# Kernel optimization log

Measured on AMD Instinct MI355X. Metric: run time of the kernel, lower is better.

The kernel has to match this reference:

```python
import jax, jax.numpy as jnp
import numpy as np

N = 100000
E = 1000000
HID = 64


def gcn_conv(x, W, b, edge_index, edge_w, num_nodes):
    # PyG GCNConv with edge_weight: add self-loops (weight 1), symmetric norm,
    # out[c] = sum_e norm_e * (x @ W)[row_e] aggregated at col_e, plus bias.
    xw = x @ W  # [N, hid]
    row = jnp.concatenate([edge_index[0], jnp.arange(num_nodes)])
    col = jnp.concatenate([edge_index[1], jnp.arange(num_nodes)])
    ew = jnp.concatenate([edge_w, jnp.ones((num_nodes,), x.dtype)])
    deg = jax.ops.segment_sum(ew, col, num_segments=num_nodes)
    dinv = jnp.where(deg > 0, jax.lax.rsqrt(deg), 0.0)
    norm = dinv[row] * ew * dinv[col]  # [E+N]
    msgs = norm[:, None] * xw[row]  # [E+N, hid]
    out = jax.ops.segment_sum(msgs, col, num_segments=num_nodes)
    return out + b


def setup_inputs() -> dict:
    key = jax.random.key(0)
    ks = jax.random.split(key, 12)
    user_x = jax.random.normal(ks[0], (N, 3), jnp.float32)
    movie_x = jax.random.normal(ks[1], (N, 18), jnp.float32)
    edge_index = jax.random.randint(ks[2], (2, E), 0, N, jnp.int64)
    edge_attr = jax.random.uniform(ks[3], (E,), jnp.float32)
    def lin(k, fan_in, fan_out):
        bound = 1.0 / np.sqrt(fan_in)
        k1, k2 = jax.random.split(k)
        W = jax.random.uniform(k1, (fan_in, fan_out), jnp.float32, -bound, bound)
        b = jax.random.uniform(k2, (fan_out,), jnp.float32, -bound, bound)
        return W, b
    W_user, b_user = lin(ks[4], 3, HID)
    W_movie, b_movie = lin(ks[5], 18, HID)
    W1, b1 = lin(ks[6], 2 * HID, 128)
    W2, b2 = lin(ks[7], 128, 1)
    return {"user_x": user_x, "movie_x": movie_x, "edge_index": edge_index,
            "edge_attr": edge_attr, "W_user": W_user, "b_user": b_user,
            "W_movie": W_movie, "b_movie": b_movie, "W1": W1, "b1": b1,
            "W2": W2, "b2": b2}


def reference(user_x, movie_x, edge_index, edge_attr, W_user, b_user,
              W_movie, b_movie, W1, b1, W2, b2):
    user_out = gcn_conv(user_x, W_user, b_user, edge_index, edge_attr, N)
    movie_out = gcn_conv(movie_x, W_movie, b_movie, edge_index, edge_attr, N)
    h = jnp.concatenate([user_out, movie_out], axis=-1)  # [N, 128]
    h = jax.nn.relu(h @ W1 + b1)
    rating_pred = h @ W2 + b2  # [N, 1]
    return rating_pred
```

## Files before the change

kernel.cpp:

```cpp
#include <hip/hip_runtime.h>
#include <hip/hip_fp16.h>

#define NN 100000
#define NE 1000000
#define BSH 7
#define BCOLS 128
#define NBUCK 782
#define SBLK 256
#define SITER 16
#define CAP 2048

__device__ __forceinline__ float2 h2f(unsigned u) {
    union { unsigned u; __half2 h; } c; c.u = u;
    return __half22float2(c.h);
}
__device__ __forceinline__ unsigned f2h2(float a, float b) {
    union { __half2 h; unsigned u; } c; c.h = __floats2half2_rn(a, b);
    return c.u;
}

#define ACC_ROW16(base)                                                      \
    {                                                                        \
        const uint4* pr_ = (const uint4*)(base);                             \
        const uint4 A_ = pr_[0];                                             \
        const uint4 B_ = pr_[1];                                             \
        const uint4 C_ = pr_[2];                                             \
        float2 f_;                                                           \
        f_ = h2f(A_.x); s21[0]  = fmaf(w, f_.x, s21[0]);  s21[1]  = fmaf(w, f_.y, s21[1]);  \
        f_ = h2f(A_.y); s21[2]  = fmaf(w, f_.x, s21[2]);  s21[3]  = fmaf(w, f_.y, s21[3]);  \
        f_ = h2f(A_.z); s21[4]  = fmaf(w, f_.x, s21[4]);  s21[5]  = fmaf(w, f_.y, s21[5]);  \
        f_ = h2f(A_.w); s21[6]  = fmaf(w, f_.x, s21[6]);  s21[7]  = fmaf(w, f_.y, s21[7]);  \
        f_ = h2f(B_.x); s21[8]  = fmaf(w, f_.x, s21[8]);  s21[9]  = fmaf(w, f_.y, s21[9]);  \
        f_ = h2f(B_.y); s21[10] = fmaf(w, f_.x, s21[10]); s21[11] = fmaf(w, f_.y, s21[11]); \
        f_ = h2f(B_.z); s21[12] = fmaf(w, f_.x, s21[12]); s21[13] = fmaf(w, f_.y, s21[13]); \
        f_ = h2f(B_.w); s21[14] = fmaf(w, f_.x, s21[14]); s21[15] = fmaf(w, f_.y, s21[15]); \
        f_ = h2f(C_.x); s21[16] = fmaf(w, f_.x, s21[16]); s21[17] = fmaf(w, f_.y, s21[17]); \
        f_ = h2f(C_.y); s21[18] = fmaf(w, f_.x, s21[18]); s21[19] = fmaf(w, f_.y, s21[19]); \
        f_ = h2f(C_.z); s21[20] = fmaf(w, f_.x, s21[20]);                    \
    }

__global__ __launch_bounds__(128) void fuse_kernel(const float* __restrict__ Wu,
                                                   const float* __restrict__ bu,
                                                   const float* __restrict__ Wm,
                                                   const float* __restrict__ bm,
                                                   const float* __restrict__ W1,
                                                   const float* __restrict__ b1,
                                                   const float* __restrict__ W2,
                                                   float* __restrict__ Mt,
                                                   int* __restrict__ cnt) {
    const int j = threadIdx.x;
    for (int i = j; i < NBUCK; i += 128) cnt[i] = 0;

    float w1c[128];
#pragma unroll
    for (int k = 0; k < 128; k++) w1c[k] = W1[k * 128 + j];

    float* row = Mt + j * 24;
#pragma unroll
    for (int m = 0; m < 3; m++) {
        float acc = 0.f;
#pragma unroll
        for (int k = 0; k < 64; k++) acc = fmaf(Wu[m * 64 + k], w1c[k], acc);
        row[m] = acc;
    }
#pragma unroll
    for (int m = 0; m < 18; m++) {
        float acc = 0.f;
#pragma unroll
        for (int k = 0; k < 64; k++) acc = fmaf(Wm[m * 64 + k], w1c[64 + k], acc);
        row[3 + m] = acc;
    }
    float bp = b1[j];
#pragma unroll
    for (int k = 0; k < 64; k++) {
        bp = fmaf(bu[k], w1c[k], bp);
        bp = fmaf(bm[k], w1c[64 + k], bp);
    }
    row[21] = bp;
    row[22] = W2[j];
    row[23] = 0.f;
}

__global__ __launch_bounds__(256) void bcnt_kernel(const int* __restrict__ col,
                                                   int* __restrict__ cnt) {
    __shared__ int h[NBUCK];
    for (int i = threadIdx.x; i < NBUCK; i += 256) h[i] = 0;
    __syncthreads();
    for (int e = blockIdx.x * 256 + threadIdx.x; e < NE; e += SBLK * 256)
        atomicAdd(&h[col[e] >> BSH], 1);
    __syncthreads();
    for (int i = threadIdx.x; i < NBUCK; i += 256)
        if (h[i]) atomicAdd(&cnt[i], h[i]);
}

__global__ __launch_bounds__(1024) void bscan_kernel(const int* __restrict__ cnt,
                                                     int* __restrict__ gbase,
                                                     int* __restrict__ H0) {
    __shared__ int s[1024];
    const int t = threadIdx.x;
    const int v = (t < NBUCK) ? cnt[t] : 0;
    s[t] = v;
    __syncthreads();
    for (int off = 1; off < 1024; off <<= 1) {
        int x = (t >= off) ? s[t - off] : 0;
        __syncthreads();
        s[t] += x;
        __syncthreads();
    }
    const int excl = s[t] - v;
    if (t < NBUCK) { gbase[t] = excl; H0[t] = excl; }
    if (t == 0) H0[NBUCK] = NE;
}

__global__ __launch_bounds__(256) void bscatter_kernel(const int* __restrict__ ei,
                                                       const float* __restrict__ ew,
                                                       int* __restrict__ gbase,
                                                       int2* __restrict__ mid) {
    __shared__ int h[NBUCK];
    __shared__ int rbase[NBUCK];
    int cs[SITER], rs[SITER];
    float wv[SITER];
    const int e0 = blockIdx.x * 256 + threadIdx.x;

    for (int i = threadIdx.x; i < NBUCK; i += 256) h[i] = 0;
    __syncthreads();
#pragma unroll
    for (int k = 0; k < SITER; k++) {
        const int e = e0 + k * (SBLK * 256);
        if (e < NE) {
            cs[k] = ei[NE + e];
            rs[k] = ei[e];
            wv[k] = ew[e];
            atomicAdd(&h[cs[k] >> BSH], 1);
        }
    }
    __syncthreads();
    for (int i = threadIdx.x; i < NBUCK; i += 256) {
        const int c0 = h[i];
        rbase[i] = c0 ? atomicAdd(&gbase[i], c0) : 0;
        h[i] = 0;
    }
    __syncthreads();
#pragma unroll
    for (int k = 0; k < SITER; k++) {
        const int e = e0 + k * (SBLK * 256);
        if (e < NE) {
            const int bb = cs[k] >> BSH;
            const int pos = rbase[bb] + atomicAdd(&h[bb], 1);
            mid[pos] = make_int2((cs[k] & (BCOLS - 1)) | (rs[k] << BSH),
                                 __float_as_int(wv[k]));
        }
    }
}

__global__ __launch_bounds__(256) void bdeg_pack_kernel(const int2* __restrict__ mid,
                                                        const int* __restrict__ H0,
                                                        const float* __restrict__ ux,
                                                        const float* __restrict__ mx,
                                                        unsigned short* __restrict__ pack16,
                                                        float* __restrict__ dinv) {
    __shared__ float dl[BCOLS];
    const int b = blockIdx.x;
    const int t = threadIdx.x;
    if (t < BCOLS) dl[t] = 0.f;
    __syncthreads();
    const int start = H0[b];
    const int end = H0[b + 1];
    for (int i = start + t; i < end; i += 256) {
        const int2 p = mid[i];
        atomicAdd(&dl[p.x & (BCOLS - 1)], __int_as_float(p.y));
    }
    __syncthreads();
    if (t < BCOLS) {
        const int r = b * BCOLS + t;
        if (r < NN) {
            const float d = rsqrtf(dl[t] + 1.0f);
            dinv[r] = d;
            float v[22];
            const float* u = ux + (size_t)r * 3;
            const float* m = mx + (size_t)r * 18;
            v[0] = d * u[0];
            v[1] = d * u[1];
            v[2] = d * u[2];
#pragma unroll
            for (int k = 0; k < 18; k++) v[3 + k] = d * m[k];
            v[21] = d;
            unsigned wb[16];
#pragma unroll
            for (int k = 0; k < 11; k++) wb[k] = f2h2(v[2 * k], v[2 * k + 1]);
#pragma unroll
            for (int k = 11; k < 16; k++) wb[k] = 0u;
            uint4* dst = (uint4*)(pack16 + (size_t)r * 32);
            dst[0] = make_uint4(wb[0], wb[1], wb[2], wb[3]);
            dst[1] = make_uint4(wb[4], wb[5], wb[6], wb[7]);
            dst[2] = make_uint4(wb[8], wb[9], wb[10], wb[11]);
            dst[3] = make_uint4(wb[12], wb[13], wb[14], wb[15]);
        }
    }
}

__global__ __launch_bounds__(256) void bagg_mlp_kernel(const int2* __restrict__ mid,
                                                       const int* __restrict__ H0,
                                                       const unsigned short* __restrict__ pack16,
                                                       const float* __restrict__ dinv,
                                                       const float* __restrict__ Mt,
                                                       const float* __restrict__ b2,
                                                       float* __restrict__ out) {
    __shared__ int2 smid[CAP];
    __shared__ int ccnt[BCOLS];
    __shared__ int cbase[BCOLS];
    __shared__ int cptr[BCOLS];
    __shared__ float sp[BCOLS][21];
    __shared__ float po[BCOLS];

    const int b = blockIdx.x;
    const int t = threadIdx.x;
    const int col = t & (BCOLS - 1);
    const int hf = t >> 7;
    const int start = H0[b];
    const int end = H0[b + 1];
    const int seg = end - start;
    const int segc = seg < CAP ? seg : CAP;

    if (t < BCOLS) ccnt[t] = 0;
    __syncthreads();
    for (int i = t; i < segc; i += 256)
        atomicAdd(&ccnt[mid[start + i].x & (BCOLS - 1)], 1);
    __syncthreads();

    if (t < 64) {
        const int a = ccnt[2 * t];
        const int bb = ccnt[2 * t + 1];
        int p = a + bb;
#pragma unroll
        for (int d = 1; d < 64; d <<= 1) {
            const int x = __shfl_up(p, d, 64);
            if (t >= d) p += x;
        }
        cbase[2 * t] = p - bb;
        cbase[2 * t + 1] = p;
        cptr[2 * t] = p - bb - a;
        cptr[2 * t + 1] = p - bb;
    }
    __syncthreads();

    for (int i = t; i < segc; i += 256) {
        const int2 p = mid[start + i];
        const int pos = atomicAdd(&cptr[p.x & (BCOLS - 1)], 1);
        smid[pos] = p;
    }
    __syncthreads();

    float s21[21];
#pragma unroll
    for (int m = 0; m < 21; m++) s21[m] = 0.f;

    const int s0 = (col == 0) ? 0 : cbase[col - 1];
    const int s1 = cbase[col];
#pragma unroll 2
    for (int i = s0 + hf; i < s1; i += 2) {
        const int2 p = smid[i];
        const unsigned row = ((unsigned)p.x) >> BSH;
        const float w = __int_as_float(p.y);
        ACC_ROW16(pack16 + (size_t)row * 32);
    }

    if (hf) {
#pragma unroll
        for (int m = 0; m < 21; m++) sp[col][m] = s21[m];
    }
    __syncthreads();

    const int c = b * BCOLS + col;
    if (!hf) {
#pragma unroll
        for (int m = 0; m < 21; m++) s21[m] += sp[col][m];
        if (seg > CAP) {
            for (int i = CAP; i < seg; i++) {
                const int2 p = mid[start + i];
                if ((p.x & (BCOLS - 1)) == col) {
                    const unsigned row = ((unsigned)p.x) >> BSH;
                    const float w = __int_as_float(p.y);
                    ACC_ROW16(pack16 + (size_t)row * 32);
                }
            }
        }
        if (c < NN) {
            const float w = 1.0f;
            ACC_ROW16(pack16 + (size_t)c * 32);
            const float d = dinv[c];
#pragma unroll
            for (int m = 0; m < 21; m++) s21[m] *= d;
        }
#pragma unroll
        for (int m = 0; m < 21; m++) sp[col][m] = s21[m];
    }
    __syncthreads();
    if (hf) {
#pragma unroll
        for (int m = 0; m < 21; m++) s21[m] = sp[col][m];
    }

    float o = 0.f;
    const int k0 = hf * 64;
#pragma unroll 4
    for (int k = k0; k < k0 + 64; k++) {
        const float* r = Mt + k * 24;
        float hsum = r[21];
#pragma unroll
        for (int m = 0; m < 21; m++) hsum = fmaf(s21[m], r[m], hsum);
        o = fmaf(fmaxf(hsum, 0.f), r[22], o);
    }
    if (hf) po[col] = o;
    __syncthreads();
    if (!hf && c < NN) out[c] = o + po[col] + b2[0];
}

extern "C" void kernel_launch(void* const* d_in, const int* in_sizes, int n_in,
                              void* d_out, int out_size, void* d_ws, size_t ws_size,
                              hipStream_t stream) {
    const float* ux = (const float*)d_in[0];
    const float* mx = (const float*)d_in[1];
    const int* ei = (const int*)d_in[2];
    const float* ew = (const float*)d_in[3];
    const float* Wu = (const float*)d_in[4];
    const float* bu = (const float*)d_in[5];
    const float* Wm = (const float*)d_in[6];
    const float* bm = (const float*)d_in[7];
    const float* W1 = (const float*)d_in[8];
    const float* b1 = (const float*)d_in[9];
    const float* W2 = (const float*)d_in[10];
    const float* b2 = (const float*)d_in[11];
    float* out = (float*)d_out;

    char* ws = (char*)d_ws;
    int*            cnt    = (int*)ws;
    int*            gbase  = (int*)(ws + 4096);
    int*            H0     = (int*)(ws + 8192);
    float*          Mt     = (float*)(ws + 12288);
    float*          dinv   = (float*)(ws + 24576);
    unsigned short* pack16 = (unsigned short*)(ws + 424576);
    int2*           mid    = (int2*)(ws + 6824576);

    fuse_kernel<<<1, 128, 0, stream>>>(Wu, bu, Wm, bm, W1, b1, W2, Mt, cnt);
    bcnt_kernel<<<SBLK, 256, 0, stream>>>(ei + NE, cnt);
    bscan_kernel<<<1, 1024, 0, stream>>>(cnt, gbase, H0);
    bscatter_kernel<<<SBLK, 256, 0, stream>>>(ei, ew, gbase, mid);
    bdeg_pack_kernel<<<NBUCK, 256, 0, stream>>>(mid, H0, ux, mx, pack16, dinv);
    bagg_mlp_kernel<<<NBUCK, 256, 0, stream>>>(mid, H0, pack16, dinv, Mt, b2, out);
}
```

Baseline: 196.8 us.

## Stage bucket scatter in shared memory and compute degrees via global atomics

The degree sum moves into the bucket-count pass as global float atomics, with zeroing done by extra blocks of the fuse kernel, so the pack kernel no longer re-reads the bucketed edge list per bucket. The scatter kernel now sorts its edges by bucket in LDS with a local prefix scan before writing, so global writes to the mid buffer are contiguous runs instead of random scattered stores. The aggregation kernel caches its edge segment in registers instead of reading it twice from global memory. The cost is a million global float atomics in the count pass and much larger LDS use in the scatter kernel, about 50 KB, which lowers its occupancy.

```diff
diff --git a/kernel.cpp b/kernel.cpp
--- a/kernel.cpp
+++ b/kernel.cpp
@@ -8,6 +8,7 @@
 #define NBUCK 782
 #define SBLK 256
 #define SITER 16
+#define SEDG (SITER * 256)
 #define CAP 2048
 
 __device__ __forceinline__ float2 h2f(unsigned u) {
@@ -39,18 +40,23 @@
         f_ = h2f(C_.z); s21[20] = fmaf(w, f_.x, s21[20]);                    \
     }
 
-__global__ __launch_bounds__(128) void fuse_kernel(const float* __restrict__ Wu,
-                                                   const float* __restrict__ bu,
-                                                   const float* __restrict__ Wm,
-                                                   const float* __restrict__ bm,
-                                                   const float* __restrict__ W1,
-                                                   const float* __restrict__ b1,
-                                                   const float* __restrict__ W2,
-                                                   float* __restrict__ Mt,
-                                                   int* __restrict__ cnt) {
+__global__ __launch_bounds__(128) void fuse_zero_kernel(const float* __restrict__ Wu,
+                                                        const float* __restrict__ bu,
+                                                        const float* __restrict__ Wm,
+                                                        const float* __restrict__ bm,
+                                                        const float* __restrict__ W1,
+                                                        const float* __restrict__ b1,
+                                                        const float* __restrict__ W2,
+                                                        float* __restrict__ Mt,
+                                                        int* __restrict__ cnt,
+                                                        float* __restrict__ degf) {
+    if (blockIdx.x != 0) {
+        const int tid = (blockIdx.x - 1) * 128 + threadIdx.x;
+        for (int i = tid; i < NBUCK; i += 256 * 128) cnt[i] = 0;
+        for (int i = tid; i < NN; i += 256 * 128) degf[i] = 0.f;
+        return;
+    }
     const int j = threadIdx.x;
-    for (int i = j; i < NBUCK; i += 128) cnt[i] = 0;
-
     float w1c[128];
 #pragma unroll
     for (int k = 0; k < 128; k++) w1c[k] = W1[k * 128 + j];
@@ -82,12 +88,17 @@
 }
 
 __global__ __launch_bounds__(256) void bcnt_kernel(const int* __restrict__ col,
-                                                   int* __restrict__ cnt) {
+                                                   const float* __restrict__ ew,
+                                                   int* __restrict__ cnt,
+                                                   float* __restrict__ degf) {
     __shared__ int h[NBUCK];
     for (int i = threadIdx.x; i < NBUCK; i += 256) h[i] = 0;
     __syncthreads();
-    for (int e = blockIdx.x * 256 + threadIdx.x; e < NE; e += SBLK * 256)
-        atomicAdd(&h[col[e] >> BSH], 1);
+    for (int e = blockIdx.x * 256 + threadIdx.x; e < NE; e += SBLK * 256) {
+        const int c = col[e];
+        atomicAdd(&h[c >> BSH], 1);
+        atomicAdd(&degf[c], ew[e]);
+    }
     __syncthreads();
     for (int i = threadIdx.x; i < NBUCK; i += 256)
         if (h[i]) atomicAdd(&cnt[i], h[i]);
@@ -116,14 +127,24 @@
                                                        const float* __restrict__ ew,
                                                        int* __restrict__ gbase,
                                                        int2* __restrict__ mid) {
+    __shared__ int2 stage[SEDG];
+    __shared__ unsigned short sbk[SEDG];
     __shared__ int h[NBUCK];
+    __shared__ int basel[NBUCK];
+    __shared__ int cptr[NBUCK];
     __shared__ int rbase[NBUCK];
+    __shared__ int wtot[4];
+    __shared__ int wpre[4];
+    __shared__ int stot;
+
     int cs[SITER], rs[SITER];
     float wv[SITER];
-    const int e0 = blockIdx.x * 256 + threadIdx.x;
-
-    for (int i = threadIdx.x; i < NBUCK; i += 256) h[i] = 0;
-    __syncthreads();
+    const int t = threadIdx.x;
+    const int e0 = blockIdx.x * 256 + t;
+
+    for (int i = t; i < NBUCK; i += 256) h[i] = 0;
+    __syncthreads();
+
 #pragma unroll
     for (int k = 0; k < SITER; k++) {
         const int e = e0 + k * (SBLK * 256);
@@ -135,68 +156,98 @@
         }
     }
     __syncthreads();
-    for (int i = threadIdx.x; i < NBUCK; i += 256) {
+
+    int loc[4];
+    int tsum = 0;
+#pragma unroll
+    for (int j = 0; j < 4; j++) {
+        const int idx = t * 4 + j;
+        const int v = (idx < NBUCK) ? h[idx] : 0;
+        loc[j] = tsum;
+        tsum += v;
+    }
+    const int lane = t & 63;
+    const int wv_id = t >> 6;
+    int incl = tsum;
+#pragma unroll
+    for (int d = 1; d < 64; d <<= 1) {
+        const int x = __shfl_up(incl, d, 64);
+        if (lane >= d) incl += x;
+    }
+    if (lane == 63) wtot[wv_id] = incl;
+    __syncthreads();
+    if (t == 0) {
+        int r = 0;
+#pragma unroll
+        for (int i = 0; i < 4; i++) { wpre[i] = r; r += wtot[i]; }
+        stot = r;
+    }
+    __syncthreads();
+    const int texcl = incl - tsum + wpre[wv_id];
+#pragma unroll
+    for (int j = 0; j < 4; j++) {
+        const int idx = t * 4 + j;
+        if (idx < NBUCK) {
+            basel[idx] = texcl + loc[j];
+            cptr[idx] = texcl + loc[j];
+        }
+    }
+    __syncthreads();
+
+    for (int i = t; i < NBUCK; i += 256) {
         const int c0 = h[i];
         rbase[i] = c0 ? atomicAdd(&gbase[i], c0) : 0;
-        h[i] = 0;
-    }
-    __syncthreads();
+    }
+    __syncthreads();
+
 #pragma unroll
     for (int k = 0; k < SITER; k++) {
         const int e = e0 + k * (SBLK * 256);
         if (e < NE) {
             const int bb = cs[k] >> BSH;
-            const int pos = rbase[bb] + atomicAdd(&h[bb], 1);
-            mid[pos] = make_int2((cs[k] & (BCOLS - 1)) | (rs[k] << BSH),
-                                 __float_as_int(wv[k]));
-        }
-    }
-}
-
-__global__ __launch_bounds__(256) void bdeg_pack_kernel(const int2* __restrict__ mid,
-                                                        const int* __restrict__ H0,
-                                                        const float* __restrict__ ux,
-                                                        const float* __restrict__ mx,
-                                                        unsigned short* __restrict__ pack16,
-                                                        float* __restrict__ dinv) {
-    __shared__ float dl[BCOLS];
-    const int b = blockIdx.x;
-    const int t = threadIdx.x;
-    if (t < BCOLS) dl[t] = 0.f;
-    __syncthreads();
-    const int start = H0[b];
-    const int end = H0[b + 1];
-    for (int i = start + t; i < end; i += 256) {
-        const int2 p = mid[i];
-        atomicAdd(&dl[p.x & (BCOLS - 1)], __int_as_float(p.y));
-    }
-    __syncthreads();
-    if (t < BCOLS) {
-        const int r = b * BCOLS + t;
-        if (r < NN) {
-            const float d = rsqrtf(dl[t] + 1.0f);
-            dinv[r] = d;
-            float v[22];
-            const float* u = ux + (size_t)r * 3;
-            const float* m = mx + (size_t)r * 18;
-            v[0] = d * u[0];
-            v[1] = d * u[1];
-            v[2] = d * u[2];
-#pragma unroll
-            for (int k = 0; k < 18; k++) v[3 + k] = d * m[k];
-            v[21] = d;
-            unsigned wb[16];
-#pragma unroll
-            for (int k = 0; k < 11; k++) wb[k] = f2h2(v[2 * k], v[2 * k + 1]);
-#pragma unroll
-            for (int k = 11; k < 16; k++) wb[k] = 0u;
-            uint4* dst = (uint4*)(pack16 + (size_t)r * 32);
-            dst[0] = make_uint4(wb[0], wb[1], wb[2], wb[3]);
-            dst[1] = make_uint4(wb[4], wb[5], wb[6], wb[7]);
-            dst[2] = make_uint4(wb[8], wb[9], wb[10], wb[11]);
-            dst[3] = make_uint4(wb[12], wb[13], wb[14], wb[15]);
-        }
-    }
+            const int pos = atomicAdd(&cptr[bb], 1);
+            stage[pos] = make_int2((cs[k] & (BCOLS - 1)) | (rs[k] << BSH),
+                                   __float_as_int(wv[k]));
+            sbk[pos] = (unsigned short)bb;
+        }
+    }
+    __syncthreads();
+
+    const int tot = stot;
+    for (int i = t; i < tot; i += 256) {
+        const int bb = sbk[i];
+        mid[rbase[bb] + (i - basel[bb])] = stage[i];
+    }
+}
+
+__global__ __launch_bounds__(256) void pack_kernel(const float* __restrict__ degf,
+                                                   const float* __restrict__ ux,
+                                                   const float* __restrict__ mx,
+                                                   unsigned short* __restrict__ pack16,
+                                                   float* __restrict__ dinv) {
+    const int r = blockIdx.x * 256 + threadIdx.x;
+    if (r >= NN) return;
+    const float d = rsqrtf(degf[r] + 1.0f);
+    dinv[r] = d;
+    float v[22];
+    const float* u = ux + (size_t)r * 3;
+    const float* m = mx + (size_t)r * 18;
+    v[0] = d * u[0];
+    v[1] = d * u[1];
+    v[2] = d * u[2];
+#pragma unroll
+    for (int k = 0; k < 18; k++) v[3 + k] = d * m[k];
+    v[21] = d;
+    unsigned wb[16];
+#pragma unroll
+    for (int k = 0; k < 11; k++) wb[k] = f2h2(v[2 * k], v[2 * k + 1]);
+#pragma unroll
+    for (int k = 11; k < 16; k++) wb[k] = 0u;
+    uint4* dst = (uint4*)(pack16 + (size_t)r * 32);
+    dst[0] = make_uint4(wb[0], wb[1], wb[2], wb[3]);
+    dst[1] = make_uint4(wb[4], wb[5], wb[6], wb[7]);
+    dst[2] = make_uint4(wb[8], wb[9], wb[10], wb[11]);
+    dst[3] = make_uint4(wb[12], wb[13], wb[14], wb[15]);
 }
 
 __global__ __launch_bounds__(256) void bagg_mlp_kernel(const int2* __restrict__ mid,
@@ -222,10 +273,17 @@
     const int seg = end - start;
     const int segc = seg < CAP ? seg : CAP;
 
+    int2 er[8];
     if (t < BCOLS) ccnt[t] = 0;
     __syncthreads();
-    for (int i = t; i < segc; i += 256)
-        atomicAdd(&ccnt[mid[start + i].x & (BCOLS - 1)], 1);
+#pragma unroll
+    for (int k = 0; k < 8; k++) {
+        const int idx = t + k * 256;
+        if (idx < segc) {
+            er[k] = mid[start + idx];
+            atomicAdd(&ccnt[er[k].x & (BCOLS - 1)], 1);
+        }
+    }
     __syncthreads();
 
     if (t < 64) {
@@ -244,10 +302,13 @@
     }
     __syncthreads();
 
-    for (int i = t; i < segc; i += 256) {
-        const int2 p = mid[start + i];
-        const int pos = atomicAdd(&cptr[p.x & (BCOLS - 1)], 1);
-        smid[pos] = p;
+#pragma unroll
+    for (int k = 0; k < 8; k++) {
+        const int idx = t + k * 256;
+        if (idx < segc) {
+            const int pos = atomicAdd(&cptr[er[k].x & (BCOLS - 1)], 1);
+            smid[pos] = er[k];
+        }
     }
     __syncthreads();
 
@@ -339,13 +400,14 @@
     int*            H0     = (int*)(ws + 8192);
     float*          Mt     = (float*)(ws + 12288);
     float*          dinv   = (float*)(ws + 24576);
-    unsigned short* pack16 = (unsigned short*)(ws + 424576);
-    int2*           mid    = (int2*)(ws + 6824576);
-
-    fuse_kernel<<<1, 128, 0, stream>>>(Wu, bu, Wm, bm, W1, b1, W2, Mt, cnt);
-    bcnt_kernel<<<SBLK, 256, 0, stream>>>(ei + NE, cnt);
+    float*          degf   = (float*)(ws + 424576);
+    unsigned short* pack16 = (unsigned short*)(ws + 824576);
+    int2*           mid    = (int2*)(ws + 7224576);
+
+    fuse_zero_kernel<<<257, 128, 0, stream>>>(Wu, bu, Wm, bm, W1, b1, W2, Mt, cnt, degf);
+    bcnt_kernel<<<SBLK, 256, 0, stream>>>(ei + NE, ew, cnt, degf);
     bscan_kernel<<<1, 1024, 0, stream>>>(cnt, gbase, H0);
     bscatter_kernel<<<SBLK, 256, 0, stream>>>(ei, ew, gbase, mid);
-    bdeg_pack_kernel<<<NBUCK, 256, 0, stream>>>(mid, H0, ux, mx, pack16, dinv);
+    pack_kernel<<<(NN + 255) / 256, 256, 0, stream>>>(degf, ux, mx, pack16, dinv);
     bagg_mlp_kernel<<<NBUCK, 256, 0, stream>>>(mid, H0, pack16, dinv, Mt, b2, out);
 }
```

Result: slower. 239.5 us (+21.7%).

## Replace count+scan bucketing with fixed-capacity buckets plus overflow list, widen aggregation

Applied to the files above, without the earlier changes.

Drops the bucket-count and prefix-scan kernels by giving each bucket a fixed slot of CAP entries, with a global overflow list for entries past capacity. The aggregate+MLP kernel now uses 512 threads with 4 lanes per column and reduces with shuffles instead of shared-memory exchanges and barriers. This removes two launches and an extra pass over the column indices. In exchange it adds overflow handling that scans the whole overflow list, and it enlarges the workspace.

```diff
diff --git a/kernel.cpp b/kernel.cpp
--- a/kernel.cpp
+++ b/kernel.cpp
@@ -9,6 +9,7 @@
 #define SBLK 256
 #define SITER 16
 #define CAP 2048
+#define OVCAP 16384
 
 __device__ __forceinline__ float2 h2f(unsigned u) {
     union { unsigned u; __half2 h; } c; c.u = u;
@@ -47,9 +48,11 @@
                                                    const float* __restrict__ b1,
                                                    const float* __restrict__ W2,
                                                    float* __restrict__ Mt,
-                                                   int* __restrict__ cnt) {
+                                                   int* __restrict__ gcur,
+                                                   int* __restrict__ ovfn) {
     const int j = threadIdx.x;
-    for (int i = j; i < NBUCK; i += 128) cnt[i] = 0;
+    for (int i = j; i < NBUCK; i += 128) gcur[i] = 0;
+    if (j == 0) *ovfn = 0;
 
     float w1c[128];
 #pragma unroll
@@ -81,41 +84,12 @@
     row[23] = 0.f;
 }
 
-__global__ __launch_bounds__(256) void bcnt_kernel(const int* __restrict__ col,
-                                                   int* __restrict__ cnt) {
-    __shared__ int h[NBUCK];
-    for (int i = threadIdx.x; i < NBUCK; i += 256) h[i] = 0;
-    __syncthreads();
-    for (int e = blockIdx.x * 256 + threadIdx.x; e < NE; e += SBLK * 256)
-        atomicAdd(&h[col[e] >> BSH], 1);
-    __syncthreads();
-    for (int i = threadIdx.x; i < NBUCK; i += 256)
-        if (h[i]) atomicAdd(&cnt[i], h[i]);
-}
-
-__global__ __launch_bounds__(1024) void bscan_kernel(const int* __restrict__ cnt,
-                                                     int* __restrict__ gbase,
-                                                     int* __restrict__ H0) {
-    __shared__ int s[1024];
-    const int t = threadIdx.x;
-    const int v = (t < NBUCK) ? cnt[t] : 0;
-    s[t] = v;
-    __syncthreads();
-    for (int off = 1; off < 1024; off <<= 1) {
-        int x = (t >= off) ? s[t - off] : 0;
-        __syncthreads();
-        s[t] += x;
-        __syncthreads();
-    }
-    const int excl = s[t] - v;
-    if (t < NBUCK) { gbase[t] = excl; H0[t] = excl; }
-    if (t == 0) H0[NBUCK] = NE;
-}
-
 __global__ __launch_bounds__(256) void bscatter_kernel(const int* __restrict__ ei,
                                                        const float* __restrict__ ew,
-                                                       int* __restrict__ gbase,
-                                                       int2* __restrict__ mid) {
+                                                       int* __restrict__ gcur,
+                                                       int2* __restrict__ mid,
+                                                       int4* __restrict__ ovf,
+                                                       int* __restrict__ ovfn) {
     __shared__ int h[NBUCK];
     __shared__ int rbase[NBUCK];
     int cs[SITER], rs[SITER];
@@ -137,7 +111,7 @@
     __syncthreads();
     for (int i = threadIdx.x; i < NBUCK; i += 256) {
         const int c0 = h[i];
-        rbase[i] = c0 ? atomicAdd(&gbase[i], c0) : 0;
+        rbase[i] = c0 ? atomicAdd(&gcur[i], c0) : 0;
         h[i] = 0;
     }
     __syncthreads();
@@ -147,14 +121,23 @@
         if (e < NE) {
             const int bb = cs[k] >> BSH;
             const int pos = rbase[bb] + atomicAdd(&h[bb], 1);
-            mid[pos] = make_int2((cs[k] & (BCOLS - 1)) | (rs[k] << BSH),
-                                 __float_as_int(wv[k]));
+            if (pos < CAP) {
+                mid[(size_t)bb * CAP + pos] =
+                    make_int2((cs[k] & (BCOLS - 1)) | (rs[k] << BSH),
+                              __float_as_int(wv[k]));
+            } else {
+                const int oi = atomicAdd(ovfn, 1);
+                if (oi < OVCAP)
+                    ovf[oi] = make_int4(cs[k], rs[k], __float_as_int(wv[k]), 0);
+            }
         }
     }
 }
 
 __global__ __launch_bounds__(256) void bdeg_pack_kernel(const int2* __restrict__ mid,
-                                                        const int* __restrict__ H0,
+                                                        const int* __restrict__ gcur,
+                                                        const int* __restrict__ ovfn,
+                                                        const int4* __restrict__ ovf,
                                                         const float* __restrict__ ux,
                                                         const float* __restrict__ mx,
                                                         unsigned short* __restrict__ pack16,
@@ -164,11 +147,20 @@
     const int t = threadIdx.x;
     if (t < BCOLS) dl[t] = 0.f;
     __syncthreads();
-    const int start = H0[b];
-    const int end = H0[b + 1];
-    for (int i = start + t; i < end; i += 256) {
-        const int2 p = mid[i];
+    const int cntt = gcur[b];
+    const int segc = cntt < CAP ? cntt : CAP;
+    const int start = b * CAP;
+    for (int i = t; i < segc; i += 256) {
+        const int2 p = mid[start + i];
         atomicAdd(&dl[p.x & (BCOLS - 1)], __int_as_float(p.y));
+    }
+    if (cntt > CAP) {
+        const int n = min(*ovfn, OVCAP);
+        for (int i = t; i < n; i += 256) {
+            const int4 q = ovf[i];
+            if ((q.x >> BSH) == b)
+                atomicAdd(&dl[q.x & (BCOLS - 1)], __int_as_float(q.z));
+        }
     }
     __syncthreads();
     if (t < BCOLS) {
@@ -199,8 +191,10 @@
     }
 }
 
-__global__ __launch_bounds__(256) void bagg_mlp_kernel(const int2* __restrict__ mid,
-                                                       const int* __restrict__ H0,
+__global__ __launch_bounds__(512) void bagg_mlp_kernel(const int2* __restrict__ mid,
+                                                       const int* __restrict__ gcur,
+                                                       const int* __restrict__ ovfn,
+                                                       const int4* __restrict__ ovf,
                                                        const unsigned short* __restrict__ pack16,
                                                        const float* __restrict__ dinv,
                                                        const float* __restrict__ Mt,
@@ -210,21 +204,18 @@
     __shared__ int ccnt[BCOLS];
     __shared__ int cbase[BCOLS];
     __shared__ int cptr[BCOLS];
-    __shared__ float sp[BCOLS][21];
-    __shared__ float po[BCOLS];
 
     const int b = blockIdx.x;
     const int t = threadIdx.x;
-    const int col = t & (BCOLS - 1);
-    const int hf = t >> 7;
-    const int start = H0[b];
-    const int end = H0[b + 1];
-    const int seg = end - start;
-    const int segc = seg < CAP ? seg : CAP;
+    const int col = t >> 2;
+    const int sub = t & 3;
+    const int start = b * CAP;
+    const int cntt = gcur[b];
+    const int segc = cntt < CAP ? cntt : CAP;
 
     if (t < BCOLS) ccnt[t] = 0;
     __syncthreads();
-    for (int i = t; i < segc; i += 256)
+    for (int i = t; i < segc; i += 512)
         atomicAdd(&ccnt[mid[start + i].x & (BCOLS - 1)], 1);
     __syncthreads();
 
@@ -244,7 +235,7 @@
     }
     __syncthreads();
 
-    for (int i = t; i < segc; i += 256) {
+    for (int i = t; i < segc; i += 512) {
         const int2 p = mid[start + i];
         const int pos = atomicAdd(&cptr[p.x & (BCOLS - 1)], 1);
         smid[pos] = p;
@@ -258,62 +249,53 @@
     const int s0 = (col == 0) ? 0 : cbase[col - 1];
     const int s1 = cbase[col];
 #pragma unroll 2
-    for (int i = s0 + hf; i < s1; i += 2) {
+    for (int i = s0 + sub; i < s1; i += 4) {
         const int2 p = smid[i];
         const unsigned row = ((unsigned)p.x) >> BSH;
         const float w = __int_as_float(p.y);
         ACC_ROW16(pack16 + (size_t)row * 32);
     }
 
-    if (hf) {
-#pragma unroll
-        for (int m = 0; m < 21; m++) sp[col][m] = s21[m];
-    }
-    __syncthreads();
-
     const int c = b * BCOLS + col;
-    if (!hf) {
-#pragma unroll
-        for (int m = 0; m < 21; m++) s21[m] += sp[col][m];
-        if (seg > CAP) {
-            for (int i = CAP; i < seg; i++) {
-                const int2 p = mid[start + i];
-                if ((p.x & (BCOLS - 1)) == col) {
-                    const unsigned row = ((unsigned)p.x) >> BSH;
-                    const float w = __int_as_float(p.y);
-                    ACC_ROW16(pack16 + (size_t)row * 32);
-                }
+    if (cntt > CAP && sub == 0 && c < NN) {
+        const int n = min(*ovfn, OVCAP);
+        for (int i = 0; i < n; i++) {
+            const int4 q = ovf[i];
+            if (q.x == c) {
+                const unsigned row = (unsigned)q.y;
+                const float w = __int_as_float(q.z);
+                ACC_ROW16(pack16 + (size_t)row * 32);
             }
         }
-        if (c < NN) {
-            const float w = 1.0f;
-            ACC_ROW16(pack16 + (size_t)c * 32);
-            const float d = dinv[c];
-#pragma unroll
-            for (int m = 0; m < 21; m++) s21[m] *= d;
-        }
-#pragma unroll
-        for (int m = 0; m < 21; m++) sp[col][m] = s21[m];
-    }
-    __syncthreads();
-    if (hf) {
-#pragma unroll
-        for (int m = 0; m < 21; m++) s21[m] = sp[col][m];
+    }
+
+#pragma unroll
+    for (int m = 0; m < 21; m++) {
+        s21[m] += __shfl_xor(s21[m], 1);
+        s21[m] += __shfl_xor(s21[m], 2);
     }
 
     float o = 0.f;
-    const int k0 = hf * 64;
-#pragma unroll 4
-    for (int k = k0; k < k0 + 64; k++) {
-        const float* r = Mt + k * 24;
-        float hsum = r[21];
-#pragma unroll
-        for (int m = 0; m < 21; m++) hsum = fmaf(s21[m], r[m], hsum);
-        o = fmaf(fmaxf(hsum, 0.f), r[22], o);
-    }
-    if (hf) po[col] = o;
-    __syncthreads();
-    if (!hf && c < NN) out[c] = o + po[col] + b2[0];
+    if (c < NN) {
+        const float w = 1.0f;
+        ACC_ROW16(pack16 + (size_t)c * 32);
+        const float d = dinv[c];
+#pragma unroll
+        for (int m = 0; m < 21; m++) s21[m] *= d;
+
+        const int k0 = sub * 32;
+#pragma unroll 2
+        for (int k = k0; k < k0 + 32; k++) {
+            const float* r = Mt + k * 24;
+            float hsum = r[21];
+#pragma unroll
+            for (int m = 0; m < 21; m++) hsum = fmaf(s21[m], r[m], hsum);
+            o = fmaf(fmaxf(hsum, 0.f), r[22], o);
+        }
+    }
+    o += __shfl_xor(o, 1);
+    o += __shfl_xor(o, 2);
+    if (sub == 0 && c < NN) out[c] = o + b2[0];
 }
 
 extern "C" void kernel_launch(void* const* d_in, const int* in_sizes, int n_in,
@@ -334,18 +316,16 @@
     float* out = (float*)d_out;
 
     char* ws = (char*)d_ws;
-    int*            cnt    = (int*)ws;
-    int*            gbase  = (int*)(ws + 4096);
-    int*            H0     = (int*)(ws + 8192);
-    float*          Mt     = (float*)(ws + 12288);
-    float*          dinv   = (float*)(ws + 24576);
-    unsigned short* pack16 = (unsigned short*)(ws + 424576);
-    int2*           mid    = (int2*)(ws + 6824576);
-
-    fuse_kernel<<<1, 128, 0, stream>>>(Wu, bu, Wm, bm, W1, b1, W2, Mt, cnt);
-    bcnt_kernel<<<SBLK, 256, 0, stream>>>(ei + NE, cnt);
-    bscan_kernel<<<1, 1024, 0, stream>>>(cnt, gbase, H0);
-    bscatter_kernel<<<SBLK, 256, 0, stream>>>(ei, ew, gbase, mid);
-    bdeg_pack_kernel<<<NBUCK, 256, 0, stream>>>(mid, H0, ux, mx, pack16, dinv);
-    bagg_mlp_kernel<<<NBUCK, 256, 0, stream>>>(mid, H0, pack16, dinv, Mt, b2, out);
-}
+    int*            gcur   = (int*)ws;
+    int*            ovfn   = (int*)(ws + 4096);
+    float*          Mt     = (float*)(ws + 8192);
+    float*          dinv   = (float*)(ws + 20480);
+    unsigned short* pack16 = (unsigned short*)(ws + 420480);
+    int2*           mid    = (int2*)(ws + 6820480);
+    int4*           ovf    = (int4*)(ws + 19632768);
+
+    fuse_kernel<<<1, 128, 0, stream>>>(Wu, bu, Wm, bm, W1, b1, W2, Mt, gcur, ovfn);
+    bscatter_kernel<<<SBLK, 256, 0, stream>>>(ei, ew, gcur, mid, ovf, ovfn);
+    bdeg_pack_kernel<<<NBUCK, 256, 0, stream>>>(mid, gcur, ovfn, ovf, ux, mx, pack16, dinv);
+    bagg_mlp_kernel<<<NBUCK, 512, 0, stream>>>(mid, gcur, ovfn, ovf, pack16, dinv, Mt, b2, out);
+}
```

Measured after the change: 312.2 us. +58.6%, slower.
